# Performance work log

Hardware: AMD Instinct MI355X
Metric: run time of the kernel (lower is better)

Reference implementation:

```python
import jax, jax.numpy as jnp
import numpy as np

ALIGN_CORNERS = True
APPLY_SMOOTHSTEP = True

SIZES = [(32, 32, 32), (64, 64, 64), (128, 128, 128), (256, 256, 256)]
FEAT_DIMS = [4, 4, 4, 4]
N_POINTS = 1048576  # 2**20 sample points (e.g. 8192 rays x 128 samples)


def setup_inputs() -> dict:
    key = jax.random.key(0)
    ks = jax.random.split(key, 1 + len(SIZES))
    # grid_sample-style coords in [-1, 1], layout [1, 1, 1, N, 3] (x, y, z)
    grid = jax.random.uniform(ks[0], (1, 1, 1, N_POINTS, 3), dtype=jnp.float32) * 2.0 - 1.0
    inp = {"grid": grid}
    for i, (size, c) in enumerate(zip(SIZES, FEAT_DIMS)):
        # original init: (rand(1,C,1,1,1)*2-1).repeat over spatial; use randn volumes for a
        # non-degenerate baseline (same shapes/math path)
        inp[f"vol{i}"] = jax.random.normal(ks[1 + i], (1, c, *size), dtype=jnp.float32)
    return inp


def _smooth_sample(vol, grid_pts):
    """Trilinear sample with border padding, align_corners=True, smoothstep weights.

    vol: [C, D, H, W]; grid_pts: [P, 3] with (x, y, z) in [-1, 1].
    Returns [C, P].
    """
    C, D, H, W = vol.shape
    # unnormalize (align_corners=True): [-1,1] -> [0, dim-1]; border padding via clip
    x = jnp.clip((grid_pts[:, 0] + 1.0) * 0.5 * (W - 1), 0.0, W - 1)
    y = jnp.clip((grid_pts[:, 1] + 1.0) * 0.5 * (H - 1), 0.0, H - 1)
    z = jnp.clip((grid_pts[:, 2] + 1.0) * 0.5 * (D - 1), 0.0, D - 1)

    x0 = jnp.floor(x); y0 = jnp.floor(y); z0 = jnp.floor(z)
    tx = x - x0; ty = y - y0; tz = z - z0
    if APPLY_SMOOTHSTEP:
        tx = tx * tx * (3.0 - 2.0 * tx)
        ty = ty * ty * (3.0 - 2.0 * ty)
        tz = tz * tz * (3.0 - 2.0 * tz)

    x0i = x0.astype(jnp.int32); x1i = jnp.minimum(x0i + 1, W - 1)
    y0i = y0.astype(jnp.int32); y1i = jnp.minimum(y0i + 1, H - 1)
    z0i = z0.astype(jnp.int32); z1i = jnp.minimum(z0i + 1, D - 1)

    # 8 corner gathers -> [C, P]
    c000 = vol[:, z0i, y0i, x0i]; c001 = vol[:, z0i, y0i, x1i]
    c010 = vol[:, z0i, y1i, x0i]; c011 = vol[:, z0i, y1i, x1i]
    c100 = vol[:, z1i, y0i, x0i]; c101 = vol[:, z1i, y0i, x1i]
    c110 = vol[:, z1i, y1i, x0i]; c111 = vol[:, z1i, y1i, x1i]

    c00 = c000 + (c001 - c000) * tx
    c01 = c010 + (c011 - c010) * tx
    c10 = c100 + (c101 - c100) * tx
    c11 = c110 + (c111 - c110) * tx
    c0 = c00 + (c01 - c00) * ty
    c1 = c10 + (c11 - c10) * ty
    return c0 + (c1 - c0) * tz


def reference(grid, vol0, vol1, vol2, vol3):
    # grid: [1, 1, 1, N, 3] -> [N, 3]
    pts = grid.reshape(-1, 3)
    n = pts.shape[0]
    out = []
    for vol in (vol0, vol1, vol2, vol3):
        feat = _smooth_sample(vol[0], pts)            # [C, N]
        out.append(feat.reshape(1, -1, 1, 1, n))      # grid_sample output layout
    return jnp.concatenate(out, axis=1)               # [1, sum(C), 1, 1, N]
```

## Files before the change

kernel.cpp:

```cpp
#include <hip/hip_runtime.h>

#define NPTS 1048576
#define NB 32
#define NBINS (NB * NB * NB)


__device__ __forceinline__ float4 lerp4(const float4 a, const float4 b, const float t) {
    return make_float4(a.x + (b.x - a.x) * t,
                       a.y + (b.y - a.y) * t,
                       a.z + (b.z - a.z) * t,
                       a.w + (b.w - a.w) * t);
}

template<int D>
__device__ __forceinline__ void coords(float g, float& t, int& i0, int& i1) {
    float x = (g + 1.0f) * (0.5f * (float)(D - 1));
    x = fminf(fmaxf(x, 0.0f), (float)(D - 1));
    float x0f = floorf(x);
    t = x - x0f;
    t = t * t * (3.0f - 2.0f * t);
    i0 = (int)x0f;
    i1 = min(i0 + 1, D - 1);
}

template<int D>
__device__ __forceinline__ float4 sample_inter(const float4* __restrict__ v,
                                               float gx, float gy, float gz) {
    float tx, ty, tz; int x0, x1, y0, y1, z0, z1;
    coords<D>(gx, tx, x0, x1);
    coords<D>(gy, ty, y0, y1);
    coords<D>(gz, tz, z0, z1);
    const int b00 = (z0 * D + y0) * D;
    const int b01 = (z0 * D + y1) * D;
    const int b10 = (z1 * D + y0) * D;
    const int b11 = (z1 * D + y1) * D;
    float4 c000 = v[b00 + x0], c001 = v[b00 + x1];
    float4 c010 = v[b01 + x0], c011 = v[b01 + x1];
    float4 c100 = v[b10 + x0], c101 = v[b10 + x1];
    float4 c110 = v[b11 + x0], c111 = v[b11 + x1];
    float4 c00 = lerp4(c000, c001, tx);
    float4 c01 = lerp4(c010, c011, tx);
    float4 c10 = lerp4(c100, c101, tx);
    float4 c11 = lerp4(c110, c111, tx);
    float4 c0 = lerp4(c00, c01, ty);
    float4 c1 = lerp4(c10, c11, ty);
    return lerp4(c0, c1, tz);
}

template<int D>
__device__ __forceinline__ float4 sample_direct(const float* __restrict__ v,
                                                float gx, float gy, float gz) {
    float tx, ty, tz; int x0, x1, y0, y1, z0, z1;
    coords<D>(gx, tx, x0, x1);
    coords<D>(gy, ty, y0, y1);
    coords<D>(gz, tz, z0, z1);
    const int b00 = (z0 * D + y0) * D;
    const int b01 = (z0 * D + y1) * D;
    const int b10 = (z1 * D + y0) * D;
    const int b11 = (z1 * D + y1) * D;
    float r[4];
#pragma unroll
    for (int c = 0; c < 4; ++c) {
        const float* __restrict__ vc = v + (size_t)c * (D * D * D);
        float c000 = vc[b00 + x0], c001 = vc[b00 + x1];
        float c010 = vc[b01 + x0], c011 = vc[b01 + x1];
        float c100 = vc[b10 + x0], c101 = vc[b10 + x1];
        float c110 = vc[b11 + x0], c111 = vc[b11 + x1];
        float c00 = c000 + (c001 - c000) * tx;
        float c01 = c010 + (c011 - c010) * tx;
        float c10 = c100 + (c101 - c100) * tx;
        float c11 = c110 + (c111 - c110) * tx;
        float c0 = c00 + (c01 - c00) * ty;
        float c1 = c10 + (c11 - c10) * ty;
        r[c] = c0 + (c1 - c0) * tz;
    }
    return make_float4(r[0], r[1], r[2], r[3]);
}


template<int DHW>
__global__ __launch_bounds__(256) void xpose_kernel(const float* __restrict__ in,
                                                    float4* __restrict__ out) {
    int v = blockIdx.x * blockDim.x + threadIdx.x;
    if (v < DHW)
        out[v] = make_float4(in[v], in[v + DHW], in[v + 2 * DHW], in[v + 3 * DHW]);
}


__device__ __forceinline__ int bin_of(float gx, float gy, float gz) {
    float ux = fminf(fmaxf((gx + 1.0f) * 0.5f, 0.0f), 1.0f);
    float uy = fminf(fmaxf((gy + 1.0f) * 0.5f, 0.0f), 1.0f);
    float uz = fminf(fmaxf((gz + 1.0f) * 0.5f, 0.0f), 1.0f);
    int bx = min((int)(ux * (float)NB), NB - 1);
    int by = min((int)(uy * (float)NB), NB - 1);
    int bz = min((int)(uz * (float)NB), NB - 1);
    return (bz * NB + by) * NB + bx;
}

__global__ __launch_bounds__(256) void bin_hist_kernel(const float* __restrict__ grid,
                                                       int* __restrict__ bins,
                                                       unsigned* __restrict__ hist) {
    int p = blockIdx.x * blockDim.x + threadIdx.x;
    float gx = grid[3 * p + 0];
    float gy = grid[3 * p + 1];
    float gz = grid[3 * p + 2];
    int b = bin_of(gx, gy, gz);
    bins[p] = b;
    atomicAdd(&hist[b], 1u);
}

__global__ __launch_bounds__(1024) void scan_kernel(const unsigned* __restrict__ hist,
                                                    unsigned* __restrict__ offsets) {
    __shared__ unsigned partial[1024];
    const int t = threadIdx.x;
    const int base = t * 32;
    unsigned sum = 0;
#pragma unroll
    for (int i = 0; i < 32; ++i) sum += hist[base + i];
    partial[t] = sum;
    __syncthreads();
    for (int off = 1; off < 1024; off <<= 1) {
        unsigned v = (t >= off) ? partial[t - off] : 0u;
        __syncthreads();
        partial[t] += v;
        __syncthreads();
    }
    unsigned run = partial[t] - sum;
#pragma unroll
    for (int i = 0; i < 32; ++i) {
        offsets[base + i] = run;
        run += hist[base + i];
    }
}

__global__ __launch_bounds__(256) void scatter_kernel(const float* __restrict__ grid,
                                                      const int* __restrict__ bins,
                                                      unsigned* __restrict__ offsets,
                                                      float4* __restrict__ sorted,
                                                      int* __restrict__ inv) {
    int p = blockIdx.x * blockDim.x + threadIdx.x;
    int b = bins[p];
    unsigned pos = atomicAdd(&offsets[b], 1u);
    float gx = grid[3 * p + 0];
    float gy = grid[3 * p + 1];
    float gz = grid[3 * p + 2];
    sorted[pos] = make_float4(gx, gy, gz, __int_as_float(p));
    inv[p] = (int)pos;
}


__global__ __launch_bounds__(256) void gather_sorted_kernel(
    const float4* __restrict__ sorted,
    const float4* __restrict__ w0, const float4* __restrict__ w1,
    const float4* __restrict__ w2, const float* __restrict__ v3,
    float4* __restrict__ wsout)
{
    int bid = blockIdx.x;
    int sb = (bid & 7) * (int)(gridDim.x >> 3) + (bid >> 3);
    int s = sb * 256 + (int)threadIdx.x;
    float4 gp = sorted[s];
    float gx = gp.x, gy = gp.y, gz = gp.z;
    float4 f0 = sample_inter<32>(w0, gx, gy, gz);
    float4 f1 = sample_inter<64>(w1, gx, gy, gz);
    float4 f2 = sample_inter<128>(w2, gx, gy, gz);
    float4 f3 = sample_direct<256>(v3, gx, gy, gz);
    float4* w = wsout + (size_t)s * 4;
    w[0] = f0; w[1] = f1; w[2] = f2; w[3] = f3;
}

__global__ __launch_bounds__(256) void permute_kernel(const float4* __restrict__ wsout,
                                                      const int* __restrict__ inv,
                                                      float* __restrict__ out) {
    int p = blockIdx.x * blockDim.x + threadIdx.x;
    int s = inv[p];
    const float4* w = wsout + (size_t)s * 4;
    float4 f0 = w[0], f1 = w[1], f2 = w[2], f3 = w[3];
    out[ 0 * NPTS + p] = f0.x; out[ 1 * NPTS + p] = f0.y;
    out[ 2 * NPTS + p] = f0.z; out[ 3 * NPTS + p] = f0.w;
    out[ 4 * NPTS + p] = f1.x; out[ 5 * NPTS + p] = f1.y;
    out[ 6 * NPTS + p] = f1.z; out[ 7 * NPTS + p] = f1.w;
    out[ 8 * NPTS + p] = f2.x; out[ 9 * NPTS + p] = f2.y;
    out[10 * NPTS + p] = f2.z; out[11 * NPTS + p] = f2.w;
    out[12 * NPTS + p] = f3.x; out[13 * NPTS + p] = f3.y;
    out[14 * NPTS + p] = f3.z; out[15 * NPTS + p] = f3.w;
}


__global__ __launch_bounds__(256) void mg_inter_kernel(
    const float* __restrict__ grid,
    const float4* __restrict__ w0, const float4* __restrict__ w1,
    const float4* __restrict__ w2, const float* __restrict__ v3,
    float* __restrict__ out)
{
    int p = blockIdx.x * blockDim.x + threadIdx.x;
    float gx = grid[3 * p + 0];
    float gy = grid[3 * p + 1];
    float gz = grid[3 * p + 2];
    float4 f0 = sample_inter<32>(w0, gx, gy, gz);
    float4 f1 = sample_inter<64>(w1, gx, gy, gz);
    float4 f2 = sample_inter<128>(w2, gx, gy, gz);
    float4 f3 = sample_direct<256>(v3, gx, gy, gz);
    out[ 0 * NPTS + p] = f0.x; out[ 1 * NPTS + p] = f0.y;
    out[ 2 * NPTS + p] = f0.z; out[ 3 * NPTS + p] = f0.w;
    out[ 4 * NPTS + p] = f1.x; out[ 5 * NPTS + p] = f1.y;
    out[ 6 * NPTS + p] = f1.z; out[ 7 * NPTS + p] = f1.w;
    out[ 8 * NPTS + p] = f2.x; out[ 9 * NPTS + p] = f2.y;
    out[10 * NPTS + p] = f2.z; out[11 * NPTS + p] = f2.w;
    out[12 * NPTS + p] = f3.x; out[13 * NPTS + p] = f3.y;
    out[14 * NPTS + p] = f3.z; out[15 * NPTS + p] = f3.w;
}

__global__ __launch_bounds__(256) void mg_direct_kernel(
    const float* __restrict__ grid,
    const float* __restrict__ v0, const float* __restrict__ v1,
    const float* __restrict__ v2, const float* __restrict__ v3,
    float* __restrict__ out)
{
    int p = blockIdx.x * blockDim.x + threadIdx.x;
    float gx = grid[3 * p + 0];
    float gy = grid[3 * p + 1];
    float gz = grid[3 * p + 2];
    float4 f0 = sample_direct<32>(v0, gx, gy, gz);
    float4 f1 = sample_direct<64>(v1, gx, gy, gz);
    float4 f2 = sample_direct<128>(v2, gx, gy, gz);
    float4 f3 = sample_direct<256>(v3, gx, gy, gz);
    out[ 0 * NPTS + p] = f0.x; out[ 1 * NPTS + p] = f0.y;
    out[ 2 * NPTS + p] = f0.z; out[ 3 * NPTS + p] = f0.w;
    out[ 4 * NPTS + p] = f1.x; out[ 5 * NPTS + p] = f1.y;
    out[ 6 * NPTS + p] = f1.z; out[ 7 * NPTS + p] = f1.w;
    out[ 8 * NPTS + p] = f2.x; out[ 9 * NPTS + p] = f2.y;
    out[10 * NPTS + p] = f2.z; out[11 * NPTS + p] = f2.w;
    out[12 * NPTS + p] = f3.x; out[13 * NPTS + p] = f3.y;
    out[14 * NPTS + p] = f3.z; out[15 * NPTS + p] = f3.w;
}


extern "C" void kernel_launch(void* const* d_in, const int* in_sizes, int n_in,
                              void* d_out, int out_size, void* d_ws, size_t ws_size,
                              hipStream_t stream) {
    const float* grid = (const float*)d_in[0];
    const float* v0   = (const float*)d_in[1];
    const float* v1   = (const float*)d_in[2];
    const float* v2   = (const float*)d_in[3];
    const float* v3   = (const float*)d_in[4];
    float* out = (float*)d_out;

    constexpr int DHW0 = 32 * 32 * 32;
    constexpr int DHW1 = 64 * 64 * 64;
    constexpr int DHW2 = 128 * 128 * 128;

    constexpr size_t OFF_WSOUT  = 0;
    constexpr size_t OFF_SORTED = OFF_WSOUT  + (size_t)NPTS * 64;
    constexpr size_t OFF_W2     = OFF_SORTED + (size_t)NPTS * 16;
    constexpr size_t OFF_W1     = OFF_W2     + (size_t)DHW2 * 16;
    constexpr size_t OFF_W0     = OFF_W1     + (size_t)DHW1 * 16;
    constexpr size_t OFF_BINS   = OFF_W0     + (size_t)DHW0 * 16;
    constexpr size_t OFF_INV    = OFF_BINS   + (size_t)NPTS * 4;
    constexpr size_t OFF_HIST   = OFF_INV    + (size_t)NPTS * 4;
    constexpr size_t OFF_OFFS   = OFF_HIST   + (size_t)NBINS * 4;
    constexpr size_t WS_FULL    = OFF_OFFS   + (size_t)NBINS * 4;
    constexpr size_t WS_INTER   = (size_t)(DHW0 + DHW1 + DHW2) * 16;

    const int threads = 256;
    const int pt_blocks = NPTS / threads;
    char* ws = (char*)d_ws;

    if (ws_size >= WS_FULL) {
        float4*   wsout  = (float4*)(ws + OFF_WSOUT);
        float4*   sorted = (float4*)(ws + OFF_SORTED);
        float4*   w2     = (float4*)(ws + OFF_W2);
        float4*   w1     = (float4*)(ws + OFF_W1);
        float4*   w0     = (float4*)(ws + OFF_W0);
        int*      bins   = (int*)   (ws + OFF_BINS);
        int*      inv    = (int*)   (ws + OFF_INV);
        unsigned* hist   = (unsigned*)(ws + OFF_HIST);
        unsigned* offs   = (unsigned*)(ws + OFF_OFFS);

        hipMemsetAsync(hist, 0, (size_t)NBINS * 4, stream);
        xpose_kernel<DHW0><<<DHW0 / threads, threads, 0, stream>>>(v0, w0);
        xpose_kernel<DHW1><<<DHW1 / threads, threads, 0, stream>>>(v1, w1);
        xpose_kernel<DHW2><<<DHW2 / threads, threads, 0, stream>>>(v2, w2);
        bin_hist_kernel<<<pt_blocks, threads, 0, stream>>>(grid, bins, hist);
        scan_kernel<<<1, 1024, 0, stream>>>(hist, offs);
        scatter_kernel<<<pt_blocks, threads, 0, stream>>>(grid, bins, offs, sorted, inv);
        gather_sorted_kernel<<<pt_blocks, threads, 0, stream>>>(sorted, w0, w1, w2, v3, wsout);
        permute_kernel<<<pt_blocks, threads, 0, stream>>>(wsout, inv, out);
    } else if (ws_size >= WS_INTER) {
        float4* w0 = (float4*)d_ws;
        float4* w1 = w0 + DHW0;
        float4* w2 = w1 + DHW1;
        xpose_kernel<DHW0><<<DHW0 / threads, threads, 0, stream>>>(v0, w0);
        xpose_kernel<DHW1><<<DHW1 / threads, threads, 0, stream>>>(v1, w1);
        xpose_kernel<DHW2><<<DHW2 / threads, threads, 0, stream>>>(v2, w2);
        mg_inter_kernel<<<pt_blocks, threads, 0, stream>>>(grid, w0, w1, w2, v3, out);
    } else {
        mg_direct_kernel<<<pt_blocks, threads, 0, stream>>>(grid, v0, v1, v2, v3, out);
    }
}
```

Before: 705.6 us.

## Batch transposes, drop bins buffer, vectorize fine-level loads, add nontemporal stores

```diff
diff --git a/kernel.cpp b/kernel.cpp
--- a/kernel.cpp
+++ b/kernel.cpp
@@ -3,6 +3,12 @@
 #define NPTS 1048576
 #define NB 32
 #define NBINS (NB * NB * NB)
+
+typedef float v4f __attribute__((ext_vector_type(4)));
+
+__device__ __forceinline__ void nt_store4(const float4& f, float4* p) {
+    __builtin_nontemporal_store(*(const v4f*)&f, (v4f*)p);
+}
 
 
 __device__ __forceinline__ float4 lerp4(const float4 a, const float4 b, const float t) {
@@ -12,78 +18,62 @@
                        a.w + (b.w - a.w) * t);
 }
 
+struct CoordW { float tx, ty, tz; int b00, b01, b10, b11, x0, x1; };
+
 template<int D>
-__device__ __forceinline__ void coords(float g, float& t, int& i0, int& i1) {
-    float x = (g + 1.0f) * (0.5f * (float)(D - 1));
-    x = fminf(fmaxf(x, 0.0f), (float)(D - 1));
-    float x0f = floorf(x);
-    t = x - x0f;
-    t = t * t * (3.0f - 2.0f * t);
-    i0 = (int)x0f;
-    i1 = min(i0 + 1, D - 1);
-}
-
-template<int D>
-__device__ __forceinline__ float4 sample_inter(const float4* __restrict__ v,
-                                               float gx, float gy, float gz) {
-    float tx, ty, tz; int x0, x1, y0, y1, z0, z1;
-    coords<D>(gx, tx, x0, x1);
-    coords<D>(gy, ty, y0, y1);
-    coords<D>(gz, tz, z0, z1);
-    const int b00 = (z0 * D + y0) * D;
-    const int b01 = (z0 * D + y1) * D;
-    const int b10 = (z1 * D + y0) * D;
-    const int b11 = (z1 * D + y1) * D;
-    float4 c000 = v[b00 + x0], c001 = v[b00 + x1];
-    float4 c010 = v[b01 + x0], c011 = v[b01 + x1];
-    float4 c100 = v[b10 + x0], c101 = v[b10 + x1];
-    float4 c110 = v[b11 + x0], c111 = v[b11 + x1];
-    float4 c00 = lerp4(c000, c001, tx);
-    float4 c01 = lerp4(c010, c011, tx);
-    float4 c10 = lerp4(c100, c101, tx);
-    float4 c11 = lerp4(c110, c111, tx);
-    float4 c0 = lerp4(c00, c01, ty);
-    float4 c1 = lerp4(c10, c11, ty);
-    return lerp4(c0, c1, tz);
-}
-
-template<int D>
-__device__ __forceinline__ float4 sample_direct(const float* __restrict__ v,
-                                                float gx, float gy, float gz) {
-    float tx, ty, tz; int x0, x1, y0, y1, z0, z1;
-    coords<D>(gx, tx, x0, x1);
-    coords<D>(gy, ty, y0, y1);
-    coords<D>(gz, tz, z0, z1);
-    const int b00 = (z0 * D + y0) * D;
-    const int b01 = (z0 * D + y1) * D;
-    const int b10 = (z1 * D + y0) * D;
-    const int b11 = (z1 * D + y1) * D;
-    float r[4];
-#pragma unroll
-    for (int c = 0; c < 4; ++c) {
-        const float* __restrict__ vc = v + (size_t)c * (D * D * D);
-        float c000 = vc[b00 + x0], c001 = vc[b00 + x1];
-        float c010 = vc[b01 + x0], c011 = vc[b01 + x1];
-        float c100 = vc[b10 + x0], c101 = vc[b10 + x1];
-        float c110 = vc[b11 + x0], c111 = vc[b11 + x1];
-        float c00 = c000 + (c001 - c000) * tx;
-        float c01 = c010 + (c011 - c010) * tx;
-        float c10 = c100 + (c101 - c100) * tx;
-        float c11 = c110 + (c111 - c110) * tx;
-        float c0 = c00 + (c01 - c00) * ty;
-        float c1 = c10 + (c11 - c10) * ty;
-        r[c] = c0 + (c1 - c0) * tz;
-    }
-    return make_float4(r[0], r[1], r[2], r[3]);
-}
-
-
-template<int DHW>
-__global__ __launch_bounds__(256) void xpose_kernel(const float* __restrict__ in,
-                                                    float4* __restrict__ out) {
-    int v = blockIdx.x * blockDim.x + threadIdx.x;
-    if (v < DHW)
-        out[v] = make_float4(in[v], in[v + DHW], in[v + 2 * DHW], in[v + 3 * DHW]);
+__device__ __forceinline__ CoordW mkcoord(float gx, float gy, float gz) {
+    CoordW c;
+    float x = fminf(fmaxf((gx + 1.0f) * (0.5f * (float)(D - 1)), 0.0f), (float)(D - 1));
+    float y = fminf(fmaxf((gy + 1.0f) * (0.5f * (float)(D - 1)), 0.0f), (float)(D - 1));
+    float z = fminf(fmaxf((gz + 1.0f) * (0.5f * (float)(D - 1)), 0.0f), (float)(D - 1));
+    float xf = floorf(x), yf = floorf(y), zf = floorf(z);
+    float tx = x - xf, ty = y - yf, tz = z - zf;
+    c.tx = tx * tx * (3.0f - 2.0f * tx);
+    c.ty = ty * ty * (3.0f - 2.0f * ty);
+    c.tz = tz * tz * (3.0f - 2.0f * tz);
+    int x0 = (int)xf, y0 = (int)yf, z0 = (int)zf;
+    int y1 = min(y0 + 1, D - 1), z1 = min(z0 + 1, D - 1);
+    c.x0 = x0;
+    c.x1 = min(x0 + 1, D - 1);
+    c.b00 = (z0 * D + y0) * D;
+    c.b01 = (z0 * D + y1) * D;
+    c.b10 = (z1 * D + y0) * D;
+    c.b11 = (z1 * D + y1) * D;
+    return c;
+}
+
+__device__ __forceinline__ float4 reduce8(const float4* q, const CoordW& c) {
+    float4 c00 = lerp4(q[0], q[1], c.tx);
+    float4 c01 = lerp4(q[2], q[3], c.tx);
+    float4 c10 = lerp4(q[4], q[5], c.tx);
+    float4 c11 = lerp4(q[6], q[7], c.tx);
+    float4 c0 = lerp4(c00, c01, c.ty);
+    float4 c1 = lerp4(c10, c11, c.ty);
+    return lerp4(c0, c1, c.tz);
+}
+
+
+#define DHW0 (32 * 32 * 32)
+#define DHW1 (64 * 64 * 64)
+#define DHW2 (128 * 128 * 128)
+
+__global__ __launch_bounds__(256) void xpose_all_kernel(
+    const float* __restrict__ v0, const float* __restrict__ v1, const float* __restrict__ v2,
+    float4* __restrict__ w0, float4* __restrict__ w1, float4* __restrict__ w2)
+{
+    constexpr int B2 = DHW2 / 256, B1 = DHW1 / 256;
+    int b = blockIdx.x;
+    int t = threadIdx.x;
+    if (b < B2) {
+        int v = b * 256 + t;
+        w2[v] = make_float4(v2[v], v2[v + DHW2], v2[v + 2 * DHW2], v2[v + 3 * DHW2]);
+    } else if (b < B2 + B1) {
+        int v = (b - B2) * 256 + t;
+        w1[v] = make_float4(v1[v], v1[v + DHW1], v1[v + 2 * DHW1], v1[v + 3 * DHW1]);
+    } else {
+        int v = (b - B2 - B1) * 256 + t;
+        w0[v] = make_float4(v0[v], v0[v + DHW0], v0[v + 2 * DHW0], v0[v + 3 * DHW0]);
+    }
 }
 
 
@@ -98,15 +88,12 @@
 }
 
 __global__ __launch_bounds__(256) void bin_hist_kernel(const float* __restrict__ grid,
-                                                       int* __restrict__ bins,
                                                        unsigned* __restrict__ hist) {
     int p = blockIdx.x * blockDim.x + threadIdx.x;
     float gx = grid[3 * p + 0];
     float gy = grid[3 * p + 1];
     float gz = grid[3 * p + 2];
-    int b = bin_of(gx, gy, gz);
-    bins[p] = b;
-    atomicAdd(&hist[b], 1u);
+    atomicAdd(&hist[bin_of(gx, gy, gz)], 1u);
 }
 
 __global__ __launch_bounds__(1024) void scan_kernel(const unsigned* __restrict__ hist,
@@ -134,22 +121,21 @@
 }
 
 __global__ __launch_bounds__(256) void scatter_kernel(const float* __restrict__ grid,
-                                                      const int* __restrict__ bins,
                                                       unsigned* __restrict__ offsets,
                                                       float4* __restrict__ sorted,
                                                       int* __restrict__ inv) {
     int p = blockIdx.x * blockDim.x + threadIdx.x;
-    int b = bins[p];
-    unsigned pos = atomicAdd(&offsets[b], 1u);
     float gx = grid[3 * p + 0];
     float gy = grid[3 * p + 1];
     float gz = grid[3 * p + 2];
+    int b = bin_of(gx, gy, gz);
+    unsigned pos = atomicAdd(&offsets[b], 1u);
     sorted[pos] = make_float4(gx, gy, gz, __int_as_float(p));
     inv[p] = (int)pos;
 }
 
 
-__global__ __launch_bounds__(256) void gather_sorted_kernel(
+__global__ __launch_bounds__(256, 4) void gather_sorted_kernel(
     const float4* __restrict__ sorted,
     const float4* __restrict__ w0, const float4* __restrict__ w1,
     const float4* __restrict__ w2, const float* __restrict__ v3,
@@ -160,21 +146,151 @@
     int s = sb * 256 + (int)threadIdx.x;
     float4 gp = sorted[s];
     float gx = gp.x, gy = gp.y, gz = gp.z;
-    float4 f0 = sample_inter<32>(w0, gx, gy, gz);
-    float4 f1 = sample_inter<64>(w1, gx, gy, gz);
-    float4 f2 = sample_inter<128>(w2, gx, gy, gz);
-    float4 f3 = sample_direct<256>(v3, gx, gy, gz);
+
+    CoordW c0 = mkcoord<32>(gx, gy, gz);
+    CoordW c1 = mkcoord<64>(gx, gy, gz);
+    CoordW c2 = mkcoord<128>(gx, gy, gz);
+    CoordW c3 = mkcoord<256>(gx, gy, gz);
+
+    float4 qa[8], qb[8], qc[8];
+    qa[0] = w0[c0.b00 + c0.x0]; qa[1] = w0[c0.b00 + c0.x1];
+    qa[2] = w0[c0.b01 + c0.x0]; qa[3] = w0[c0.b01 + c0.x1];
+    qa[4] = w0[c0.b10 + c0.x0]; qa[5] = w0[c0.b10 + c0.x1];
+    qa[6] = w0[c0.b11 + c0.x0]; qa[7] = w0[c0.b11 + c0.x1];
+
+    qb[0] = w1[c1.b00 + c1.x0]; qb[1] = w1[c1.b00 + c1.x1];
+    qb[2] = w1[c1.b01 + c1.x0]; qb[3] = w1[c1.b01 + c1.x1];
+    qb[4] = w1[c1.b10 + c1.x0]; qb[5] = w1[c1.b10 + c1.x1];
+    qb[6] = w1[c1.b11 + c1.x0]; qb[7] = w1[c1.b11 + c1.x1];
+
+    qc[0] = w2[c2.b00 + c2.x0]; qc[1] = w2[c2.b00 + c2.x1];
+    qc[2] = w2[c2.b01 + c2.x0]; qc[3] = w2[c2.b01 + c2.x1];
+    qc[4] = w2[c2.b10 + c2.x0]; qc[5] = w2[c2.b10 + c2.x1];
+    qc[6] = w2[c2.b11 + c2.x0]; qc[7] = w2[c2.b11 + c2.x1];
+
+    const int xm = min(c3.x0, 254);
+    const bool edge = (c3.x0 == 255);
+    float2 qd[16];
+#pragma unroll
+    for (int ch = 0; ch < 4; ++ch) {
+        const float* __restrict__ vc = v3 + (size_t)ch * (256 * 256 * 256);
+        qd[ch * 4 + 0] = *(const float2*)(vc + c3.b00 + xm);
+        qd[ch * 4 + 1] = *(const float2*)(vc + c3.b01 + xm);
+        qd[ch * 4 + 2] = *(const float2*)(vc + c3.b10 + xm);
+        qd[ch * 4 + 3] = *(const float2*)(vc + c3.b11 + xm);
+    }
+
+    float4 f0 = reduce8(qa, c0);
+    float4 f1 = reduce8(qb, c1);
+    float4 f2 = reduce8(qc, c2);
+
+    float r3[4];
+#pragma unroll
+    for (int ch = 0; ch < 4; ++ch) {
+        float v00a = edge ? qd[ch * 4 + 0].y : qd[ch * 4 + 0].x, v00b = qd[ch * 4 + 0].y;
+        float v01a = edge ? qd[ch * 4 + 1].y : qd[ch * 4 + 1].x, v01b = qd[ch * 4 + 1].y;
+        float v10a = edge ? qd[ch * 4 + 2].y : qd[ch * 4 + 2].x, v10b = qd[ch * 4 + 2].y;
+        float v11a = edge ? qd[ch * 4 + 3].y : qd[ch * 4 + 3].x, v11b = qd[ch * 4 + 3].y;
+        float c00 = v00a + (v00b - v00a) * c3.tx;
+        float c01 = v01a + (v01b - v01a) * c3.tx;
+        float c10 = v10a + (v10b - v10a) * c3.tx;
+        float c11 = v11a + (v11b - v11a) * c3.tx;
+        float e0 = c00 + (c01 - c00) * c3.ty;
+        float e1 = c10 + (c11 - c10) * c3.ty;
+        r3[ch] = e0 + (e1 - e0) * c3.tz;
+    }
+    float4 f3 = make_float4(r3[0], r3[1], r3[2], r3[3]);
+
     float4* w = wsout + (size_t)s * 4;
-    w[0] = f0; w[1] = f1; w[2] = f2; w[3] = f3;
+    nt_store4(f0, w + 0);
+    nt_store4(f1, w + 1);
+    nt_store4(f2, w + 2);
+    nt_store4(f3, w + 3);
+}
+
+
+__device__ __forceinline__ void permute_one(const float4* __restrict__ wsout,
+                                            const int* __restrict__ inv,
+                                            float* __restrict__ out, int p) {
+    int s = inv[p];
+    const float4* w = wsout + (size_t)s * 4;
+    float4 f0 = w[0], f1 = w[1], f2 = w[2], f3 = w[3];
+    __builtin_nontemporal_store(f0.x, &out[ 0 * NPTS + p]);
+    __builtin_nontemporal_store(f0.y, &out[ 1 * NPTS + p]);
+    __builtin_nontemporal_store(f0.z, &out[ 2 * NPTS + p]);
+    __builtin_nontemporal_store(f0.w, &out[ 3 * NPTS + p]);
+    __builtin_nontemporal_store(f1.x, &out[ 4 * NPTS + p]);
+    __builtin_nontemporal_store(f1.y, &out[ 5 * NPTS + p]);
+    __builtin_nontemporal_store(f1.z, &out[ 6 * NPTS + p]);
+    __builtin_nontemporal_store(f1.w, &out[ 7 * NPTS + p]);
+    __builtin_nontemporal_store(f2.x, &out[ 8 * NPTS + p]);
+    __builtin_nontemporal_store(f2.y, &out[ 9 * NPTS + p]);
+    __builtin_nontemporal_store(f2.z, &out[10 * NPTS + p]);
+    __builtin_nontemporal_store(f2.w, &out[11 * NPTS + p]);
+    __builtin_nontemporal_store(f3.x, &out[12 * NPTS + p]);
+    __builtin_nontemporal_store(f3.y, &out[13 * NPTS + p]);
+    __builtin_nontemporal_store(f3.z, &out[14 * NPTS + p]);
+    __builtin_nontemporal_store(f3.w, &out[15 * NPTS + p]);
 }
 
 __global__ __launch_bounds__(256) void permute_kernel(const float4* __restrict__ wsout,
                                                       const int* __restrict__ inv,
                                                       float* __restrict__ out) {
     int p = blockIdx.x * blockDim.x + threadIdx.x;
-    int s = inv[p];
-    const float4* w = wsout + (size_t)s * 4;
-    float4 f0 = w[0], f1 = w[1], f2 = w[2], f3 = w[3];
+    permute_one(wsout, inv, out, p);
+    permute_one(wsout, inv, out, p + NPTS / 2);
+}
+
+
+template<int D>
+__device__ __forceinline__ float4 sample_inter(const float4* __restrict__ v,
+                                               float gx, float gy, float gz) {
+    CoordW c = mkcoord<D>(gx, gy, gz);
+    float4 q[8];
+    q[0] = v[c.b00 + c.x0]; q[1] = v[c.b00 + c.x1];
+    q[2] = v[c.b01 + c.x0]; q[3] = v[c.b01 + c.x1];
+    q[4] = v[c.b10 + c.x0]; q[5] = v[c.b10 + c.x1];
+    q[6] = v[c.b11 + c.x0]; q[7] = v[c.b11 + c.x1];
+    return reduce8(q, c);
+}
+
+template<int D>
+__device__ __forceinline__ float4 sample_direct(const float* __restrict__ v,
+                                                float gx, float gy, float gz) {
+    CoordW c = mkcoord<D>(gx, gy, gz);
+    float r[4];
+#pragma unroll
+    for (int ch = 0; ch < 4; ++ch) {
+        const float* __restrict__ vc = v + (size_t)ch * (D * D * D);
+        float c000 = vc[c.b00 + c.x0], c001 = vc[c.b00 + c.x1];
+        float c010 = vc[c.b01 + c.x0], c011 = vc[c.b01 + c.x1];
+        float c100 = vc[c.b10 + c.x0], c101 = vc[c.b10 + c.x1];
+        float c110 = vc[c.b11 + c.x0], c111 = vc[c.b11 + c.x1];
+        float c00 = c000 + (c001 - c000) * c.tx;
+        float c01 = c010 + (c011 - c010) * c.tx;
+        float c10 = c100 + (c101 - c100) * c.tx;
+        float c11 = c110 + (c111 - c110) * c.tx;
+        float e0 = c00 + (c01 - c00) * c.ty;
+        float e1 = c10 + (c11 - c10) * c.ty;
+        r[ch] = e0 + (e1 - e0) * c.tz;
+    }
+    return make_float4(r[0], r[1], r[2], r[3]);
+}
+
+__global__ __launch_bounds__(256) void mg_direct_kernel(
+    const float* __restrict__ grid,
+    const float* __restrict__ v0, const float* __restrict__ v1,
+    const float* __restrict__ v2, const float* __restrict__ v3,
+    float* __restrict__ out)
+{
+    int p = blockIdx.x * blockDim.x + threadIdx.x;
+    float gx = grid[3 * p + 0];
+    float gy = grid[3 * p + 1];
+    float gz = grid[3 * p + 2];
+    float4 f0 = sample_direct<32>(v0, gx, gy, gz);
+    float4 f1 = sample_direct<64>(v1, gx, gy, gz);
+    float4 f2 = sample_direct<128>(v2, gx, gy, gz);
+    float4 f3 = sample_direct<256>(v3, gx, gy, gz);
     out[ 0 * NPTS + p] = f0.x; out[ 1 * NPTS + p] = f0.y;
     out[ 2 * NPTS + p] = f0.z; out[ 3 * NPTS + p] = f0.w;
     out[ 4 * NPTS + p] = f1.x; out[ 5 * NPTS + p] = f1.y;
@@ -184,7 +300,6 @@
     out[12 * NPTS + p] = f3.x; out[13 * NPTS + p] = f3.y;
     out[14 * NPTS + p] = f3.z; out[15 * NPTS + p] = f3.w;
 }
-
 
 __global__ __launch_bounds__(256) void mg_inter_kernel(
     const float* __restrict__ grid,
@@ -210,30 +325,6 @@
     out[14 * NPTS + p] = f3.z; out[15 * NPTS + p] = f3.w;
 }
 
-__global__ __launch_bounds__(256) void mg_direct_kernel(
-    const float* __restrict__ grid,
-    const float* __restrict__ v0, const float* __restrict__ v1,
-    const float* __restrict__ v2, const float* __restrict__ v3,
-    float* __restrict__ out)
-{
-    int p = blockIdx.x * blockDim.x + threadIdx.x;
-    float gx = grid[3 * p + 0];
-    float gy = grid[3 * p + 1];
-    float gz = grid[3 * p + 2];
-    float4 f0 = sample_direct<32>(v0, gx, gy, gz);
-    float4 f1 = sample_direct<64>(v1, gx, gy, gz);
-    float4 f2 = sample_direct<128>(v2, gx, gy, gz);
-    float4 f3 = sample_direct<256>(v3, gx, gy, gz);
-    out[ 0 * NPTS + p] = f0.x; out[ 1 * NPTS + p] = f0.y;
-    out[ 2 * NPTS + p] = f0.z; out[ 3 * NPTS + p] = f0.w;
-    out[ 4 * NPTS + p] = f1.x; out[ 5 * NPTS + p] = f1.y;
-    out[ 6 * NPTS + p] = f1.z; out[ 7 * NPTS + p] = f1.w;
-    out[ 8 * NPTS + p] = f2.x; out[ 9 * NPTS + p] = f2.y;
-    out[10 * NPTS + p] = f2.z; out[11 * NPTS + p] = f2.w;
-    out[12 * NPTS + p] = f3.x; out[13 * NPTS + p] = f3.y;
-    out[14 * NPTS + p] = f3.z; out[15 * NPTS + p] = f3.w;
-}
-
 
 extern "C" void kernel_launch(void* const* d_in, const int* in_sizes, int n_in,
                               void* d_out, int out_size, void* d_ws, size_t ws_size,
@@ -245,17 +336,12 @@
     const float* v3   = (const float*)d_in[4];
     float* out = (float*)d_out;
 
-    constexpr int DHW0 = 32 * 32 * 32;
-    constexpr int DHW1 = 64 * 64 * 64;
-    constexpr int DHW2 = 128 * 128 * 128;
-
     constexpr size_t OFF_WSOUT  = 0;
     constexpr size_t OFF_SORTED = OFF_WSOUT  + (size_t)NPTS * 64;
     constexpr size_t OFF_W2     = OFF_SORTED + (size_t)NPTS * 16;
     constexpr size_t OFF_W1     = OFF_W2     + (size_t)DHW2 * 16;
     constexpr size_t OFF_W0     = OFF_W1     + (size_t)DHW1 * 16;
-    constexpr size_t OFF_BINS   = OFF_W0     + (size_t)DHW0 * 16;
-    constexpr size_t OFF_INV    = OFF_BINS   + (size_t)NPTS * 4;
+    constexpr size_t OFF_INV    = OFF_W0     + (size_t)DHW0 * 16;
     constexpr size_t OFF_HIST   = OFF_INV    + (size_t)NPTS * 4;
     constexpr size_t OFF_OFFS   = OFF_HIST   + (size_t)NBINS * 4;
     constexpr size_t WS_FULL    = OFF_OFFS   + (size_t)NBINS * 4;
@@ -271,27 +357,24 @@
         float4*   w2     = (float4*)(ws + OFF_W2);
         float4*   w1     = (float4*)(ws + OFF_W1);
         float4*   w0     = (float4*)(ws + OFF_W0);
-        int*      bins   = (int*)   (ws + OFF_BINS);
         int*      inv    = (int*)   (ws + OFF_INV);
         unsigned* hist   = (unsigned*)(ws + OFF_HIST);
         unsigned* offs   = (unsigned*)(ws + OFF_OFFS);
 
-        hipMemsetAsync(hist, 0, (size_t)NBINS * 4, stream);
-        xpose_kernel<DHW0><<<DHW0 / threads, threads, 0, stream>>>(v0, w0);
-        xpose_kernel<DHW1><<<DHW1 / threads, threads, 0, stream>>>(v1, w1);
-        xpose_kernel<DHW2><<<DHW2 / threads, threads, 0, stream>>>(v2, w2);
-        bin_hist_kernel<<<pt_blocks, threads, 0, stream>>>(grid, bins, hist);
+        (void)hipMemsetAsync(hist, 0, (size_t)NBINS * 4, stream);
+        xpose_all_kernel<<<(DHW0 + DHW1 + DHW2) / threads, threads, 0, stream>>>(
+            v0, v1, v2, w0, w1, w2);
+        bin_hist_kernel<<<pt_blocks, threads, 0, stream>>>(grid, hist);
         scan_kernel<<<1, 1024, 0, stream>>>(hist, offs);
-        scatter_kernel<<<pt_blocks, threads, 0, stream>>>(grid, bins, offs, sorted, inv);
+        scatter_kernel<<<pt_blocks, threads, 0, stream>>>(grid, offs, sorted, inv);
         gather_sorted_kernel<<<pt_blocks, threads, 0, stream>>>(sorted, w0, w1, w2, v3, wsout);
-        permute_kernel<<<pt_blocks, threads, 0, stream>>>(wsout, inv, out);
+        permute_kernel<<<pt_blocks / 2, threads, 0, stream>>>(wsout, inv, out);
     } else if (ws_size >= WS_INTER) {
         float4* w0 = (float4*)d_ws;
         float4* w1 = w0 + DHW0;
         float4* w2 = w1 + DHW1;
-        xpose_kernel<DHW0><<<DHW0 / threads, threads, 0, stream>>>(v0, w0);
-        xpose_kernel<DHW1><<<DHW1 / threads, threads, 0, stream>>>(v1, w1);
-        xpose_kernel<DHW2><<<DHW2 / threads, threads, 0, stream>>>(v2, w2);
+        xpose_all_kernel<<<(DHW0 + DHW1 + DHW2) / threads, threads, 0, stream>>>(
+            v0, v1, v2, w0, w1, w2);
         mg_inter_kernel<<<pt_blocks, threads, 0, stream>>>(grid, w0, w1, w2, v3, out);
     } else {
         mg_direct_kernel<<<pt_blocks, threads, 0, stream>>>(grid, v0, v1, v2, v3, out);
```

New measurement: 660.4 us. 6.4% less time.
